# Kernel tuning notes

Measured on AMD Instinct MI355X. Metric: run time of the kernel, lower is better.

Reference implementation:

```python
import jax, jax.numpy as jnp
import numpy as np

N_NODES = 50000


def gcn_conv(x, row, col, ew, W, b, n_nodes):
    """PyG GCNConv: add self-loops, symmetric normalization, scatter-add aggregation."""
    loop = jnp.arange(n_nodes)
    r = jnp.concatenate([row, loop])
    c = jnp.concatenate([col, loop])
    w = jnp.concatenate([ew, jnp.ones((n_nodes,), ew.dtype)])
    deg = jax.ops.segment_sum(w, c, num_segments=n_nodes)          # [N]
    dinv = jnp.where(deg > 0, jax.lax.rsqrt(deg), 0.0)
    norm = dinv[r] * w * dinv[c]                                   # [E+N]
    h = x @ W                                                      # [N, out]
    msg = h[r] * norm[:, None]                                     # [E+N, out]
    out = jax.ops.segment_sum(msg, c, num_segments=n_nodes)        # [N, out]
    return out + b


def setup_inputs() -> dict:
    key = jax.random.key(0)
    ks = jax.random.split(key, 7)
    n_feats, hidden, n_classes, n_edges = 256, 128, 40, 800000
    x = jax.random.normal(ks[0], (N_NODES, n_feats), dtype=jnp.float32)
    edge_index = jax.random.randint(ks[1], (2, n_edges), 0, N_NODES, dtype=jnp.int64)
    edge_weight = jax.random.uniform(ks[2], (n_edges,), dtype=jnp.float32)
    # Glorot-ish init for the two GCNConv linear layers (weight stored as [in, out])
    W1 = jax.random.normal(ks[3], (n_feats, hidden), dtype=jnp.float32) * (1.0 / np.sqrt(n_feats))
    b1 = jnp.zeros((hidden,), dtype=jnp.float32)
    W2 = jax.random.normal(ks[4], (hidden, n_classes), dtype=jnp.float32) * (1.0 / np.sqrt(hidden))
    b2 = jnp.zeros((n_classes,), dtype=jnp.float32)
    return {"x": x, "edge_index": edge_index, "edge_weight": edge_weight,
            "W1": W1, "b1": b1, "W2": W2, "b2": b2}


def reference(x, edge_index, edge_weight, W1, b1, W2, b2):
    # Dropout is identity in eval mode.
    row, col = edge_index[0], edge_index[1]
    h = gcn_conv(x, row, col, edge_weight, W1, b1, N_NODES)
    h = jax.nn.relu(h)
    out = gcn_conv(h, row, col, edge_weight, W2, b2, N_NODES)
    return out
```

## Files before the change

### kernel.cpp

```cpp
#include <hip/hip_runtime.h>

#define N_FEATS 256
#define HIDDEN  128
#define NCLASS  40
#define H2PAD   48
#define ELLCAP  64

typedef __attribute__((ext_vector_type(8))) short short8;
typedef __attribute__((ext_vector_type(4))) float f32x4;

static __device__ __forceinline__ unsigned short f2bf(float f) {
    unsigned u = __float_as_uint(f);
    u += 0x7fffu + ((u >> 16) & 1u);
    return (unsigned short)(u >> 16);
}
static __device__ __forceinline__ float bflo(unsigned u) { return __uint_as_float(u << 16); }
static __device__ __forceinline__ float bfhi(unsigned u) { return __uint_as_float(u & 0xffff0000u); }

static __device__ __forceinline__ unsigned wq16(float w) {
    float q = w * 65536.0f + 0.5f;
    q = fminf(q, 65535.0f);
    return (unsigned)q;
}
#define WDEQ (1.0f / 65536.0f)

__global__ void k_convW(const float* __restrict__ W1, const float* __restrict__ W2,
                        unsigned short* __restrict__ Wp, unsigned short* __restrict__ Wp2,
                        unsigned long long* __restrict__ cntw, int N) {
    int idx = blockIdx.x * 256 + threadIdx.x;
    if (idx < N) cntw[idx] = 0ull;
    if (idx < N_FEATS * HIDDEN) {
        int n = idx >> 8, k = idx & 255;
        Wp[idx] = f2bf(W1[(size_t)k * HIDDEN + n]);
    } else {
        int j = idx - N_FEATS * HIDDEN;
        if (j < H2PAD * HIDDEN) {
            int n = j >> 7, k = j & 127;
            Wp2[j] = (n < NCLASS) ? f2bf(W2[(size_t)k * NCLASS + n]) : 0;
        }
    }
}

__global__ __launch_bounds__(256) void k_fat(const float* __restrict__ x,
                                             const unsigned short* __restrict__ Wp,
                                             unsigned short* __restrict__ C,
                                             const int* __restrict__ col,
                                             const int* __restrict__ row,
                                             const float* __restrict__ ew,
                                             unsigned long long* __restrict__ cntw,
                                             unsigned* __restrict__ ed,
                                             int GB, int CB, int N, int E) {
    int bid = blockIdx.x;
    int M = GB < CB ? GB : CB;
    int tile = -1, chunk = -1;
    if (bid < 2 * M) {
        if (bid & 1) chunk = bid >> 1; else tile = bid >> 1;
    } else {
        int r = bid - 2 * M;
        if (GB > CB) tile = M + r; else chunk = M + r;
    }

    if (tile >= 0) {
        __shared__ unsigned short Als[64][72];
        __shared__ unsigned short Bls[128][72];
        int t = threadIdx.x;
        int r0 = tile * 64;
        int wave = t >> 6, lane = t & 63;
        int ml = lane & 15, qd = lane >> 4;

        f32x4 acc[8];
        #pragma unroll
        for (int i = 0; i < 8; ++i) acc[i] = (f32x4){0.f, 0.f, 0.f, 0.f};

        int arow = t >> 2, akg = t & 3;
        int bn = t >> 1, bkg = t & 1;

        for (int k0 = 0; k0 < N_FEATS; k0 += 32) {
            {
                float4 xa0 = make_float4(0.f, 0.f, 0.f, 0.f), xa1 = xa0;
                if (r0 + arow < N) {
                    const float* src = &x[(size_t)(r0 + arow) * N_FEATS + k0 + akg * 8];
                    xa0 = *(const float4*)src;
                    xa1 = *(const float4*)(src + 4);
                }
                short8 av;
                av[0] = (short)f2bf(xa0.x); av[1] = (short)f2bf(xa0.y);
                av[2] = (short)f2bf(xa0.z); av[3] = (short)f2bf(xa0.w);
                av[4] = (short)f2bf(xa1.x); av[5] = (short)f2bf(xa1.y);
                av[6] = (short)f2bf(xa1.z); av[7] = (short)f2bf(xa1.w);
                *(short8*)&Als[arow][akg * 8] = av;
            }
            {
                const short8* src = (const short8*)&Wp[(size_t)bn * N_FEATS + k0 + bkg * 16];
                *(short8*)&Bls[bn][bkg * 16]     = src[0];
                *(short8*)&Bls[bn][bkg * 16 + 8] = src[1];
            }
            __syncthreads();
            short8 af = *(const short8*)&Als[wave * 16 + ml][qd * 8];
            #pragma unroll
            for (int nt = 0; nt < 8; ++nt) {
                short8 bf = *(const short8*)&Bls[nt * 16 + ml][qd * 8];
                acc[nt] = __builtin_amdgcn_mfma_f32_16x16x32_bf16(af, bf, acc[nt], 0, 0, 0);
            }
            __syncthreads();
        }
        #pragma unroll
        for (int nt = 0; nt < 8; ++nt) {
            #pragma unroll
            for (int r = 0; r < 4; ++r) {
                int grow = r0 + wave * 16 + qd * 4 + r;
                if (grow < N)
                    C[(size_t)grow * HIDDEN + nt * 16 + ml] = (unsigned short)f2bf(acc[nt][r]);
            }
        }
    } else {
        int base = chunk * 1024 + threadIdx.x * 4;
        if (base + 4 <= E) {
            int4   c4 = *(const int4*)&col[base];
            int4   r4 = *(const int4*)&row[base];
            float4 w4 = *(const float4*)&ew[base];
            unsigned q0 = wq16(w4.x), q1 = wq16(w4.y), q2 = wq16(w4.z), q3 = wq16(w4.w);
            unsigned p0 = ((unsigned)r4.x << 16) | q0;
            unsigned p1 = ((unsigned)r4.y << 16) | q1;
            unsigned p2 = ((unsigned)r4.z << 16) | q2;
            unsigned p3 = ((unsigned)r4.w << 16) | q3;
            unsigned long long a0 = atomicAdd(&cntw[c4.x], ((unsigned long long)q0 << 20) | 1ull);
            unsigned long long a1 = atomicAdd(&cntw[c4.y], ((unsigned long long)q1 << 20) | 1ull);
            unsigned long long a2 = atomicAdd(&cntw[c4.z], ((unsigned long long)q2 << 20) | 1ull);
            unsigned long long a3 = atomicAdd(&cntw[c4.w], ((unsigned long long)q3 << 20) | 1ull);
            int s0 = (int)(a0 & 0xFFFFFu);
            int s1 = (int)(a1 & 0xFFFFFu);
            int s2 = (int)(a2 & 0xFFFFFu);
            int s3 = (int)(a3 & 0xFFFFFu);
            if (s0 < ELLCAP) __builtin_nontemporal_store(p0, &ed[((size_t)c4.x << 6) + s0]);
            if (s1 < ELLCAP) __builtin_nontemporal_store(p1, &ed[((size_t)c4.y << 6) + s1]);
            if (s2 < ELLCAP) __builtin_nontemporal_store(p2, &ed[((size_t)c4.z << 6) + s2]);
            if (s3 < ELLCAP) __builtin_nontemporal_store(p3, &ed[((size_t)c4.w << 6) + s3]);
        } else {
            for (int e = base; e < E; ++e) {
                int c = col[e];
                unsigned q = wq16(ew[e]);
                unsigned p = ((unsigned)row[e] << 16) | q;
                unsigned long long a = atomicAdd(&cntw[c], ((unsigned long long)q << 20) | 1ull);
                int s = (int)(a & 0xFFFFFu);
                if (s < ELLCAP) __builtin_nontemporal_store(p, &ed[((size_t)c << 6) + s]);
            }
        }
    }
}

__global__ void k_degdinv(const unsigned long long* __restrict__ cntw,
                          float* __restrict__ dinv, int* __restrict__ cnt, int N) {
    int c = blockIdx.x * blockDim.x + threadIdx.x;
    if (c >= N) return;
    unsigned long long v = cntw[c];
    int m = (int)(v & 0xFFFFFu); if (m > ELLCAP) m = ELLCAP;
    cnt[c] = m;
    dinv[c] = rsqrtf(1.0f + (float)(v >> 20) * WDEQ);
}

__global__ __launch_bounds__(1024) void k_gather1(const int* __restrict__ cnt,
                                                  const unsigned* __restrict__ ed,
                                                  const unsigned short* __restrict__ h,
                                                  const float* __restrict__ dinv,
                                                  const float* __restrict__ b1,
                                                  const unsigned short* __restrict__ Wp2,
                                                  unsigned short* __restrict__ h2b, int N) {
    __shared__ unsigned short Ah[16][136];
    int t = threadIdx.x;
    int wave = t >> 6, lane = t & 63;
    int g = lane >> 4, f = lane & 15;
    int c0 = blockIdx.x * 16;
    int c = c0 + wave;
    const uint4* hb = (const uint4*)h;

    float acc[8] = {};
    short8 ov = {};
    if (c < N) {
        int m = cnt[c];
        const unsigned* ep = ed + ((size_t)c << 6);
        int i = 0;
        for (; i + 8 <= m; i += 8) {
            unsigned e0 = ep[i + g], e1 = ep[i + g + 4];
            uint4 v0 = hb[(size_t)(e0 >> 16) * 16 + f];
            uint4 v1 = hb[(size_t)(e1 >> 16) * 16 + f];
            float w0 = (float)(e0 & 0xffffu) * WDEQ * dinv[e0 >> 16];
            float w1 = (float)(e1 & 0xffffu) * WDEQ * dinv[e1 >> 16];
            acc[0] += w0 * bflo(v0.x); acc[1] += w0 * bfhi(v0.x);
            acc[2] += w0 * bflo(v0.y); acc[3] += w0 * bfhi(v0.y);
            acc[4] += w0 * bflo(v0.z); acc[5] += w0 * bfhi(v0.z);
            acc[6] += w0 * bflo(v0.w); acc[7] += w0 * bfhi(v0.w);
            acc[0] += w1 * bflo(v1.x); acc[1] += w1 * bfhi(v1.x);
            acc[2] += w1 * bflo(v1.y); acc[3] += w1 * bfhi(v1.y);
            acc[4] += w1 * bflo(v1.z); acc[5] += w1 * bfhi(v1.z);
            acc[6] += w1 * bflo(v1.w); acc[7] += w1 * bfhi(v1.w);
        }
        if (i + g < m) {
            unsigned e0 = ep[i + g];
            uint4 v0 = hb[(size_t)(e0 >> 16) * 16 + f];
            float w0 = (float)(e0 & 0xffffu) * WDEQ * dinv[e0 >> 16];
            acc[0] += w0 * bflo(v0.x); acc[1] += w0 * bfhi(v0.x);
            acc[2] += w0 * bflo(v0.y); acc[3] += w0 * bfhi(v0.y);
            acc[4] += w0 * bflo(v0.z); acc[5] += w0 * bfhi(v0.z);
            acc[6] += w0 * bflo(v0.w); acc[7] += w0 * bfhi(v0.w);
        }
        if (i + g + 4 < m) {
            unsigned e1 = ep[i + g + 4];
            uint4 v1 = hb[(size_t)(e1 >> 16) * 16 + f];
            float w1 = (float)(e1 & 0xffffu) * WDEQ * dinv[e1 >> 16];
            acc[0] += w1 * bflo(v1.x); acc[1] += w1 * bfhi(v1.x);
            acc[2] += w1 * bflo(v1.y); acc[3] += w1 * bfhi(v1.y);
            acc[4] += w1 * bflo(v1.z); acc[5] += w1 * bfhi(v1.z);
            acc[6] += w1 * bflo(v1.w); acc[7] += w1 * bfhi(v1.w);
        }
        #pragma unroll
        for (int j = 0; j < 8; ++j) acc[j] += __shfl_xor(acc[j], 16, 64);
        #pragma unroll
        for (int j = 0; j < 8; ++j) acc[j] += __shfl_xor(acc[j], 32, 64);

        float dc = dinv[c], sl = dc * dc;
        uint4 hv = hb[(size_t)c * 16 + f];
        float4 ba = *(const float4*)&b1[f * 8];
        float4 bb = *(const float4*)&b1[f * 8 + 4];
        float o[8];
        o[0] = dc * acc[0] + sl * bflo(hv.x) + ba.x;
        o[1] = dc * acc[1] + sl * bfhi(hv.x) + ba.y;
        o[2] = dc * acc[2] + sl * bflo(hv.y) + ba.z;
        o[3] = dc * acc[3] + sl * bfhi(hv.y) + ba.w;
        o[4] = dc * acc[4] + sl * bflo(hv.z) + bb.x;
        o[5] = dc * acc[5] + sl * bfhi(hv.z) + bb.y;
        o[6] = dc * acc[6] + sl * bflo(hv.w) + bb.z;
        o[7] = dc * acc[7] + sl * bfhi(hv.w) + bb.w;
        #pragma unroll
        for (int j = 0; j < 8; ++j) {
            float v = o[j] > 0.f ? o[j] : 0.f;
            ov[j] = (short)f2bf(v);
        }
    }
    if (g == 0) *(short8*)&Ah[wave][f * 8] = ov;
    __syncthreads();

    if (t < 64) {
        int ml = t & 15, qd = t >> 4;
        f32x4 acc2[3];
        #pragma unroll
        for (int i = 0; i < 3; ++i) acc2[i] = (f32x4){0.f, 0.f, 0.f, 0.f};
        #pragma unroll
        for (int ks = 0; ks < 4; ++ks) {
            short8 af = *(const short8*)&Ah[ml][ks * 32 + qd * 8];
            #pragma unroll
            for (int nt = 0; nt < 3; ++nt) {
                short8 bf = *(const short8*)&Wp2[(size_t)(nt * 16 + ml) * HIDDEN + ks * 32 + qd * 8];
                acc2[nt] = __builtin_amdgcn_mfma_f32_16x16x32_bf16(af, bf, acc2[nt], 0, 0, 0);
            }
        }
        #pragma unroll
        for (int nt = 0; nt < 3; ++nt) {
            int j = nt * 16 + ml;
            #pragma unroll
            for (int r = 0; r < 4; ++r) {
                int gr = c0 + qd * 4 + r;
                if (gr < N) h2b[(size_t)gr * H2PAD + j] = (unsigned short)f2bf(acc2[nt][r]);
            }
        }
    }
}

__global__ __launch_bounds__(256) void k_gather2(const int* __restrict__ cnt,
                                                 const unsigned* __restrict__ ed,
                                                 const unsigned short* __restrict__ h,
                                                 const float* __restrict__ dinv,
                                                 const float* __restrict__ b2,
                                                 float* __restrict__ out, int N) {
    int t = threadIdx.x;
    int wave = t >> 6, lane = t & 63;
    int g = lane >> 3, s = lane & 7;
    int c = blockIdx.x * 4 + wave;
    if (c >= N) return;
    const uint4* hb = (const uint4*)h;
    bool act = s < 6;
    int m = cnt[c];
    const unsigned* ep = ed + ((size_t)c << 6);
    float acc[8] = {};
    int i = 0;
    for (; i + 16 <= m; i += 16) {
        unsigned e0 = ep[i + g], e1 = ep[i + g + 8];
        float w0 = (float)(e0 & 0xffffu) * WDEQ * dinv[e0 >> 16];
        float w1 = (float)(e1 & 0xffffu) * WDEQ * dinv[e1 >> 16];
        if (act) {
            uint4 v0 = hb[(size_t)(e0 >> 16) * 6 + s];
            uint4 v1 = hb[(size_t)(e1 >> 16) * 6 + s];
            acc[0] += w0 * bflo(v0.x); acc[1] += w0 * bfhi(v0.x);
            acc[2] += w0 * bflo(v0.y); acc[3] += w0 * bfhi(v0.y);
            acc[4] += w0 * bflo(v0.z); acc[5] += w0 * bfhi(v0.z);
            acc[6] += w0 * bflo(v0.w); acc[7] += w0 * bfhi(v0.w);
            acc[0] += w1 * bflo(v1.x); acc[1] += w1 * bfhi(v1.x);
            acc[2] += w1 * bflo(v1.y); acc[3] += w1 * bfhi(v1.y);
            acc[4] += w1 * bflo(v1.z); acc[5] += w1 * bfhi(v1.z);
            acc[6] += w1 * bflo(v1.w); acc[7] += w1 * bfhi(v1.w);
        }
    }
    if (i + g < m) {
        unsigned e0 = ep[i + g];
        float w0 = (float)(e0 & 0xffffu) * WDEQ * dinv[e0 >> 16];
        if (act) {
            uint4 v0 = hb[(size_t)(e0 >> 16) * 6 + s];
            acc[0] += w0 * bflo(v0.x); acc[1] += w0 * bfhi(v0.x);
            acc[2] += w0 * bflo(v0.y); acc[3] += w0 * bfhi(v0.y);
            acc[4] += w0 * bflo(v0.z); acc[5] += w0 * bfhi(v0.z);
            acc[6] += w0 * bflo(v0.w); acc[7] += w0 * bfhi(v0.w);
        }
    }
    if (i + g + 8 < m) {
        unsigned e1 = ep[i + g + 8];
        float w1 = (float)(e1 & 0xffffu) * WDEQ * dinv[e1 >> 16];
        if (act) {
            uint4 v1 = hb[(size_t)(e1 >> 16) * 6 + s];
            acc[0] += w1 * bflo(v1.x); acc[1] += w1 * bfhi(v1.x);
            acc[2] += w1 * bflo(v1.y); acc[3] += w1 * bfhi(v1.y);
            acc[4] += w1 * bflo(v1.z); acc[5] += w1 * bfhi(v1.z);
            acc[6] += w1 * bflo(v1.w); acc[7] += w1 * bfhi(v1.w);
        }
    }
    #pragma unroll
    for (int j = 0; j < 8; ++j) acc[j] += __shfl_xor(acc[j], 8, 64);
    #pragma unroll
    for (int j = 0; j < 8; ++j) acc[j] += __shfl_xor(acc[j], 16, 64);
    #pragma unroll
    for (int j = 0; j < 8; ++j) acc[j] += __shfl_xor(acc[j], 32, 64);

    if (g == 0 && s < 5) {
        float dc = dinv[c], sl = dc * dc;
        uint4 hv = hb[(size_t)c * 6 + s];
        float4 ba = *(const float4*)&b2[s * 8];
        float4 bb = *(const float4*)&b2[s * 8 + 4];
        float4 oa, ob;
        oa.x = dc * acc[0] + sl * bflo(hv.x) + ba.x;
        oa.y = dc * acc[1] + sl * bfhi(hv.x) + ba.y;
        oa.z = dc * acc[2] + sl * bflo(hv.y) + ba.z;
        oa.w = dc * acc[3] + sl * bfhi(hv.y) + ba.w;
        ob.x = dc * acc[4] + sl * bflo(hv.z) + bb.x;
        ob.y = dc * acc[5] + sl * bfhi(hv.z) + bb.y;
        ob.z = dc * acc[6] + sl * bflo(hv.w) + bb.z;
        ob.w = dc * acc[7] + sl * bfhi(hv.w) + bb.w;
        *(float4*)&out[(size_t)c * NCLASS + s * 8]     = oa;
        *(float4*)&out[(size_t)c * NCLASS + s * 8 + 4] = ob;
    }
}

extern "C" void kernel_launch(void* const* d_in, const int* in_sizes, int n_in,
                              void* d_out, int out_size, void* d_ws, size_t ws_size,
                              hipStream_t stream) {
    const float* x  = (const float*)d_in[0];
    const int*   ei = (const int*)d_in[1];
    const float* ew = (const float*)d_in[2];
    const float* W1 = (const float*)d_in[3];
    const float* b1 = (const float*)d_in[4];
    const float* W2 = (const float*)d_in[5];
    const float* b2 = (const float*)d_in[6];
    float* out = (float*)d_out;

    const int E = in_sizes[2];
    const int N = in_sizes[0] / N_FEATS;
    const int* row = ei;
    const int* col = ei + E;

    unsigned long long* cntw = (unsigned long long*)d_ws;
    float* dinv = (float*)(cntw + N);
    int*   cnt  = (int*)(dinv + N);
    unsigned* ed = (unsigned*)(cnt + N);
    unsigned short* Wp  = (unsigned short*)(ed + (size_t)N * ELLCAP);
    unsigned short* Wp2 = Wp + (size_t)N_FEATS * HIDDEN;
    unsigned short* h1b = Wp2 + H2PAD * HIDDEN;
    unsigned short* h2b = h1b + (size_t)N * HIDDEN;

    {
        int nw = N_FEATS * HIDDEN + H2PAD * HIDDEN;
        int total = N > nw ? N : nw;
        k_convW<<<(total + 255) / 256, 256, 0, stream>>>(W1, W2, Wp, Wp2, cntw, N);
    }

    {
        int GB = (N + 63) / 64;
        int CB = (E + 1023) / 1024;
        k_fat<<<GB + CB, 256, 0, stream>>>(x, Wp, h1b, col, row, ew, cntw, ed, GB, CB, N, E);
    }

    k_degdinv<<<(N + 255) / 256, 256, 0, stream>>>(cntw, dinv, cnt, N);

    k_gather1<<<(N + 15) / 16, 1024, 0, stream>>>(cnt, ed, h1b, dinv, b1, Wp2, h2b, N);

    k_gather2<<<(N + 3) / 4, 256, 0, stream>>>(cnt, ed, h2b, dinv, b2, out, N);
}
```

Baseline: 204.1 us.

## Store h1 in four 32-feature slabs and gather slab-wise with 4 nodes per wave

The first-layer GEMM output is now stored feature-blocked: four contiguous slabs of 32 bf16 features per node instead of one row of 128. The gather kernel drops from 1024 to 256 threads per block. Each wave handles 4 nodes, 16 lanes each, and loops over the four slabs so each pass gathers from a smaller working set that fits better in cache. The trade-off is four passes over the edge list per node instead of one, plus narrower 64-byte row fetches.

```diff
diff --git a/kernel.cpp b/kernel.cpp
--- a/kernel.cpp
+++ b/kernel.cpp
@@ -106,11 +106,13 @@
         }
         #pragma unroll
         for (int nt = 0; nt < 8; ++nt) {
+            int q = nt >> 1;
+            int fo = (nt & 1) * 16 + ml;
             #pragma unroll
             for (int r = 0; r < 4; ++r) {
                 int grow = r0 + wave * 16 + qd * 4 + r;
                 if (grow < N)
-                    C[(size_t)grow * HIDDEN + nt * 16 + ml] = (unsigned short)f2bf(acc[nt][r]);
+                    C[(size_t)q * N * 32 + (size_t)grow * 32 + fo] = (unsigned short)f2bf(acc[nt][r]);
             }
         }
     } else {
@@ -159,31 +161,40 @@
     dinv[c] = rsqrtf(1.0f + (float)(v >> 20) * WDEQ);
 }
 
-__global__ __launch_bounds__(1024) void k_gather1(const int* __restrict__ cnt,
-                                                  const unsigned* __restrict__ ed,
-                                                  const unsigned short* __restrict__ h,
-                                                  const float* __restrict__ dinv,
-                                                  const float* __restrict__ b1,
-                                                  const unsigned short* __restrict__ Wp2,
-                                                  unsigned short* __restrict__ h2b, int N) {
+__global__ __launch_bounds__(256) void k_gather1(const int* __restrict__ cnt,
+                                                 const unsigned* __restrict__ ed,
+                                                 const unsigned short* __restrict__ h,
+                                                 const float* __restrict__ dinv,
+                                                 const float* __restrict__ b1,
+                                                 const unsigned short* __restrict__ Wp2,
+                                                 unsigned short* __restrict__ h2b, int N) {
     __shared__ unsigned short Ah[16][136];
     int t = threadIdx.x;
     int wave = t >> 6, lane = t & 63;
-    int g = lane >> 4, f = lane & 15;
+    int nl = lane >> 4;
+    int sub = lane & 15;
+    int g = sub >> 2;
+    int f2 = sub & 3;
     int c0 = blockIdx.x * 16;
-    int c = c0 + wave;
+    int node = wave * 4 + nl;
+    int c = c0 + node;
     const uint4* hb = (const uint4*)h;
 
-    float acc[8] = {};
-    short8 ov = {};
-    if (c < N) {
-        int m = cnt[c];
-        const unsigned* ep = ed + ((size_t)c << 6);
+    bool valid = c < N;
+    int m = valid ? cnt[c] : 0;
+    const unsigned* ep = ed + ((size_t)c << 6);
+    float dc = valid ? dinv[c] : 0.f;
+    float sl = dc * dc;
+
+    #pragma unroll
+    for (int q = 0; q < 4; ++q) {
+        const uint4* hq = hb + (size_t)q * N * 4;
+        float acc[8] = {};
         int i = 0;
         for (; i + 8 <= m; i += 8) {
-            unsigned e0 = ep[i + g], e1 = ep[i + g + 4];
-            uint4 v0 = hb[(size_t)(e0 >> 16) * 16 + f];
-            uint4 v1 = hb[(size_t)(e1 >> 16) * 16 + f];
+            unsigned e0 = ep[i + g], e1 = ep[i + 4 + g];
+            uint4 v0 = hq[(size_t)(e0 >> 16) * 4 + f2];
+            uint4 v1 = hq[(size_t)(e1 >> 16) * 4 + f2];
             float w0 = (float)(e0 & 0xffffu) * WDEQ * dinv[e0 >> 16];
             float w1 = (float)(e1 & 0xffffu) * WDEQ * dinv[e1 >> 16];
             acc[0] += w0 * bflo(v0.x); acc[1] += w0 * bfhi(v0.x);
@@ -197,16 +208,16 @@
         }
         if (i + g < m) {
             unsigned e0 = ep[i + g];
-            uint4 v0 = hb[(size_t)(e0 >> 16) * 16 + f];
+            uint4 v0 = hq[(size_t)(e0 >> 16) * 4 + f2];
             float w0 = (float)(e0 & 0xffffu) * WDEQ * dinv[e0 >> 16];
             acc[0] += w0 * bflo(v0.x); acc[1] += w0 * bfhi(v0.x);
             acc[2] += w0 * bflo(v0.y); acc[3] += w0 * bfhi(v0.y);
             acc[4] += w0 * bflo(v0.z); acc[5] += w0 * bfhi(v0.z);
             acc[6] += w0 * bflo(v0.w); acc[7] += w0 * bfhi(v0.w);
         }
-        if (i + g + 4 < m) {
-            unsigned e1 = ep[i + g + 4];
-            uint4 v1 = hb[(size_t)(e1 >> 16) * 16 + f];
+        if (i + 4 + g < m) {
+            unsigned e1 = ep[i + 4 + g];
+            uint4 v1 = hq[(size_t)(e1 >> 16) * 4 + f2];
             float w1 = (float)(e1 & 0xffffu) * WDEQ * dinv[e1 >> 16];
             acc[0] += w1 * bflo(v1.x); acc[1] += w1 * bfhi(v1.x);
             acc[2] += w1 * bflo(v1.y); acc[3] += w1 * bfhi(v1.y);
@@ -214,30 +225,32 @@
             acc[6] += w1 * bflo(v1.w); acc[7] += w1 * bfhi(v1.w);
         }
         #pragma unroll
-        for (int j = 0; j < 8; ++j) acc[j] += __shfl_xor(acc[j], 16, 64);
-        #pragma unroll
-        for (int j = 0; j < 8; ++j) acc[j] += __shfl_xor(acc[j], 32, 64);
-
-        float dc = dinv[c], sl = dc * dc;
-        uint4 hv = hb[(size_t)c * 16 + f];
-        float4 ba = *(const float4*)&b1[f * 8];
-        float4 bb = *(const float4*)&b1[f * 8 + 4];
-        float o[8];
-        o[0] = dc * acc[0] + sl * bflo(hv.x) + ba.x;
-        o[1] = dc * acc[1] + sl * bfhi(hv.x) + ba.y;
-        o[2] = dc * acc[2] + sl * bflo(hv.y) + ba.z;
-        o[3] = dc * acc[3] + sl * bfhi(hv.y) + ba.w;
-        o[4] = dc * acc[4] + sl * bflo(hv.z) + bb.x;
-        o[5] = dc * acc[5] + sl * bfhi(hv.z) + bb.y;
-        o[6] = dc * acc[6] + sl * bflo(hv.w) + bb.z;
-        o[7] = dc * acc[7] + sl * bfhi(hv.w) + bb.w;
-        #pragma unroll
-        for (int j = 0; j < 8; ++j) {
-            float v = o[j] > 0.f ? o[j] : 0.f;
-            ov[j] = (short)f2bf(v);
-        }
-    }
-    if (g == 0) *(short8*)&Ah[wave][f * 8] = ov;
+        for (int j = 0; j < 8; ++j) acc[j] += __shfl_xor(acc[j], 4, 64);
+        #pragma unroll
+        for (int j = 0; j < 8; ++j) acc[j] += __shfl_xor(acc[j], 8, 64);
+
+        short8 ov = {};
+        if (valid) {
+            uint4 hv = hq[(size_t)c * 4 + f2];
+            float4 ba = *(const float4*)&b1[q * 32 + f2 * 8];
+            float4 bb = *(const float4*)&b1[q * 32 + f2 * 8 + 4];
+            float o[8];
+            o[0] = dc * acc[0] + sl * bflo(hv.x) + ba.x;
+            o[1] = dc * acc[1] + sl * bfhi(hv.x) + ba.y;
+            o[2] = dc * acc[2] + sl * bflo(hv.y) + ba.z;
+            o[3] = dc * acc[3] + sl * bfhi(hv.y) + ba.w;
+            o[4] = dc * acc[4] + sl * bflo(hv.z) + bb.x;
+            o[5] = dc * acc[5] + sl * bfhi(hv.z) + bb.y;
+            o[6] = dc * acc[6] + sl * bflo(hv.w) + bb.z;
+            o[7] = dc * acc[7] + sl * bfhi(hv.w) + bb.w;
+            #pragma unroll
+            for (int j = 0; j < 8; ++j) {
+                float v = o[j] > 0.f ? o[j] : 0.f;
+                ov[j] = (short)f2bf(v);
+            }
+        }
+        if (g == 0) *(short8*)&Ah[node][q * 32 + f2 * 8] = ov;
+    }
     __syncthreads();
 
     if (t < 64) {
@@ -388,7 +401,7 @@
 
     k_degdinv<<<(N + 255) / 256, 256, 0, stream>>>(cntw, dinv, cnt, N);
 
-    k_gather1<<<(N + 15) / 16, 1024, 0, stream>>>(cnt, ed, h1b, dinv, b1, Wp2, h2b, N);
+    k_gather1<<<(N + 15) / 16, 256, 0, stream>>>(cnt, ed, h1b, dinv, b1, Wp2, h2b, N);
 
     k_gather2<<<(N + 3) / 4, 256, 0, stream>>>(cnt, ed, h2b, dinv, b2, out, N);
 }
```

Result: slower. 213.4 us (+4.6%).
